# Kernel tuning notes

Measured on AMD Instinct MI355X. Metric: run time of the kernel, lower is better.

## Reference

```python
import jax, jax.numpy as jnp
import numpy as np

C = 256
INTER = C // 8  # 32

def setup_inputs() -> dict:
    key = jax.random.key(0)
    ks = jax.random.split(key, 7)
    B, H, W = 8, 64, 64
    x = jax.random.normal(ks[0], (B, C, H, W), dtype=jnp.float32)
    # 1x1 convs == per-pixel linear maps
    Wq = jax.random.normal(ks[1], (INTER, C), dtype=jnp.float32) * (1.0 / np.sqrt(C))
    bq = jnp.zeros((INTER,), dtype=jnp.float32)
    Wk = jax.random.normal(ks[2], (INTER, C), dtype=jnp.float32) * (1.0 / np.sqrt(C))
    bk = jnp.zeros((INTER,), dtype=jnp.float32)
    Wv = jax.random.normal(ks[3], (C, C), dtype=jnp.float32) * (1.0 / np.sqrt(C))
    bv = jnp.zeros((C,), dtype=jnp.float32)
    gamma = jnp.asarray([0.1], dtype=jnp.float32)  # nonzero so attention path matters
    return {"x": x, "Wq": Wq, "bq": bq, "Wk": Wk, "bk": bk, "Wv": Wv, "bv": bv, "gamma": gamma}

def reference(x, Wq, bq, Wk, bk, Wv, bv, gamma):
    B, Cc, H, W = x.shape
    N = H * W
    xf = x.reshape(B, Cc, N)  # [B, C, N]
    # 1x1 conv projections (per-pixel linear)
    q = jnp.einsum('ic,bcn->bni', Wq, xf) + bq[None, None, :]   # [B, N, inter]
    k = jnp.einsum('ic,bcn->bin', Wk, xf) + bk[None, :, None]   # [B, inter, N]
    v = jnp.einsum('oc,bcn->bon', Wv, xf) + bv[None, :, None]   # [B, C, N]
    energy = jnp.einsum('bni,bim->bnm', q, k)                   # [B, N, N], unscaled
    attn = jax.nn.softmax(energy, axis=-1)                      # softmax over keys
    # out[b,c,i] = sum_j v[b,c,j] * attn[b,i,j]
    out = jnp.einsum('bcj,bij->bci', v, attn).reshape(B, Cc, H, W)
    return gamma[0] * out + x
```

## Files before the change

### kernel.cpp

```cpp
#include <hip/hip_runtime.h>
#include <hip/hip_bf16.h>

#define CCH 256
#define NPIX 4096
#define NB 8
#define LOG2E 1.4426950408889634f

typedef __attribute__((ext_vector_type(8))) short bf16x8;
typedef __attribute__((ext_vector_type(16))) float f32x16;

typedef __attribute__((address_space(3))) unsigned lds_u32;
typedef const __attribute__((address_space(1))) unsigned glb_u32;
#define GL_LDS16(gp, lp) \
    __builtin_amdgcn_global_load_lds((glb_u32*)(gp), (lds_u32*)(lp), 16, 0, 0)

#define PBAR() do { __builtin_amdgcn_sched_barrier(0); \
    asm volatile("s_waitcnt vmcnt(0) lgkmcnt(0)" ::: "memory"); \
    __builtin_amdgcn_s_barrier(); __builtin_amdgcn_sched_barrier(0); } while (0)

static __device__ __forceinline__ unsigned pkbf(float a, float b) {
    union { __hip_bfloat16 h[2]; unsigned u; } p;
    p.h[0] = __float2bfloat16(a);
    p.h[1] = __float2bfloat16(b);
    return p.u;
}
static __device__ __forceinline__ unsigned short bf1(float a) {
    union { __hip_bfloat16 h; unsigned short s; } p;
    p.h = __float2bfloat16(a);
    return p.s;
}

__global__ void packw_kernel(const float* __restrict__ Wq,
                             const float* __restrict__ Wk,
                             const float* __restrict__ Wv,
                             unsigned short* __restrict__ Wb) {
    int i4 = blockIdx.x * 256 + threadIdx.x;
    if (i4 >= 20480) return;
    int e = i4 * 4;
    const float* src;
    if (e < 8192)       src = Wq + e;
    else if (e < 16384) src = Wk + (e - 8192);
    else                src = Wv + (e - 16384);
    float4 v = *(const float4*)src;
    uint2 o;
    o.x = pkbf(v.x, v.y);
    o.y = pkbf(v.z, v.w);
    *(uint2*)(Wb + e) = o;
}

__global__ __launch_bounds__(320) void qkv_kernel(
    const float* __restrict__ x,
    const unsigned short* __restrict__ Wb,
    const float* __restrict__ bq, const float* __restrict__ bk,
    const float* __restrict__ bv,
    unsigned short* __restrict__ q, unsigned short* __restrict__ k,
    unsigned short* __restrict__ v)
{
    __shared__ __align__(16) unsigned xp[128][36];

    const int t   = threadIdx.x;
    const int b   = blockIdx.x >> 7;
    const int px0 = (blockIdx.x & 127) * 32;

    const float4* gx = (const float4*)x + ((size_t)b * CCH * NPIX + px0) / 4;
    for (int i = t; i < 1024; i += 320) {
        int kp = i >> 3, p4 = i & 7;
        float4 lo = gx[(size_t)(2 * kp) * (NPIX / 4) + p4];
        float4 hi = gx[(size_t)(2 * kp + 1) * (NPIX / 4) + p4];
        uint4 pk4;
        pk4.x = pkbf(lo.x, hi.x);
        pk4.y = pkbf(lo.y, hi.y);
        pk4.z = pkbf(lo.z, hi.z);
        pk4.w = pkbf(lo.w, hi.w);
        *(uint4*)&xp[kp][p4 * 4] = pk4;
    }
    __syncthreads();

    const int w  = t >> 6;
    const int lane = t & 63;
    const int qi = lane & 31, h = lane >> 5;

    f32x16 acc[2];
    #pragma unroll
    for (int rt = 0; rt < 2; ++rt)
        #pragma unroll
        for (int r = 0; r < 16; ++r) acc[rt][r] = 0.f;

    #pragma unroll 4
    for (int ks = 0; ks < 16; ++ks) {
        union { unsigned uw[4]; bf16x8 v8; } xb;
        #pragma unroll
        for (int j = 0; j < 4; ++j) xb.uw[j] = xp[ks * 8 + 4 * h + j][qi];
        #pragma unroll
        for (int rt = 0; rt < 2; ++rt) {
            int row = (2 * w + rt) * 32 + qi;
            bf16x8 af = *(const bf16x8*)(Wb + (size_t)row * 256 + ks * 16 + h * 8);
            acc[rt] = __builtin_amdgcn_mfma_f32_32x32x16_bf16(af, xb.v8, acc[rt], 0, 0, 0);
        }
    }

    const int px = px0 + qi;
    const int pxv = px0 + ((qi & 19) | ((qi & 4) << 1) | ((qi & 8) >> 1));
    #pragma unroll
    for (int rt = 0; rt < 2; ++rt) {
        int tile = 2 * w + rt;
        if (tile < 2) {
            const float* bias = (tile == 0) ? bq : bk;
            unsigned short* outp = (tile == 0) ? q : k;
            float scale = (tile == 0) ? LOG2E : 1.0f;
            #pragma unroll
            for (int rg = 0; rg < 4; ++rg) {
                float vv[4];
                #pragma unroll
                for (int j = 0; j < 4; ++j) {
                    int outd = j + 8 * rg + 4 * h;
                    vv[j] = (acc[rt][4 * rg + j] + bias[outd]) * scale;
                }
                uint2 st;
                st.x = pkbf(vv[0], vv[1]);
                st.y = pkbf(vv[2], vv[3]);
                *(uint2*)(outp + ((size_t)b * NPIX + px) * 32 + 8 * rg + 4 * h) = st;
            }
        } else {
            #pragma unroll
            for (int r = 0; r < 16; ++r) {
                int outd = (r & 3) + 8 * (r >> 2) + 4 * h;
                int grow = (tile - 2) * 32 + outd;
                v[((size_t)b * CCH + grow) * NPIX + pxv] = bf1(acc[rt][r] + bv[grow]);
            }
        }
    }
}

__global__ __launch_bounds__(512, 2) void attn_kernel(
    const unsigned short* __restrict__ qg,
    const unsigned short* __restrict__ kg,
    const unsigned short* __restrict__ vg,
    const float* __restrict__ x,
    const float* __restrict__ gamma,
    float* __restrict__ out)
{
    __shared__ __align__(16) unsigned short Kl[2][64][4][8];
    __shared__ __align__(16) unsigned short Vl[2][256][8][8];
    __shared__ __align__(16) unsigned short Pt[2][128][72];
    __shared__ float Lx[128];

    const int t    = threadIdx.x;
    const int b    = blockIdx.x & 7;
    const int n0   = (blockIdx.x >> 3) * 128;
    const int w    = t >> 6;
    const int lane = t & 63;
    const int qi = lane & 31, h = lane >> 5;

    if (w < 4) {
        const int qt = w;
        bf16x8 qf0, qf1;
        {
            const unsigned short* qp = qg + ((size_t)b * NPIX + n0 + qt * 32 + qi) * 32;
            qf0 = *(const bf16x8*)(qp + h * 8);
            qf1 = *(const bf16x8*)(qp + 16 + h * 8);
        }
        const int srow = t >> 2;
        const unsigned short* kg_src =
            kg + ((size_t)b * NPIX + srow) * 32 + ((t & 3) ^ (srow & 3)) * 8;
        char* kl_dst = (char*)Kl + t * 16;
        const unsigned short* krd[2][2];
        #pragma unroll
        for (int sub = 0; sub < 2; ++sub)
            #pragma unroll
            for (int s = 0; s < 2; ++s)
                krd[sub][s] = &Kl[0][sub * 32 + qi][(2 * s + h) ^ (qi & 3)][0];
        unsigned short* pw_base = &Pt[0][32 * qt + qi][4 * h];

        float l_run = 0.f;

        auto STAGEK = [&](int buf, int kt) {
            GL_LDS16(kg_src + (size_t)kt * 2048, kl_dst + buf * 4096);
        };
        auto QKSM = [&](int kt) {
            const int kb = kt & 1;
            f32x16 s0, s1;
            #pragma unroll
            for (int r = 0; r < 16; ++r) { s0[r] = 0.f; s1[r] = 0.f; }
            s0 = __builtin_amdgcn_mfma_f32_32x32x16_bf16(*(const bf16x8*)(krd[0][0] + kb * 2048), qf0, s0, 0, 0, 0);
            s0 = __builtin_amdgcn_mfma_f32_32x32x16_bf16(*(const bf16x8*)(krd[0][1] + kb * 2048), qf1, s0, 0, 0, 0);
            s1 = __builtin_amdgcn_mfma_f32_32x32x16_bf16(*(const bf16x8*)(krd[1][0] + kb * 2048), qf0, s1, 0, 0, 0);
            s1 = __builtin_amdgcn_mfma_f32_32x32x16_bf16(*(const bf16x8*)(krd[1][1] + kb * 2048), qf1, s1, 0, 0, 0);
            unsigned short* pw = pw_base + (kt & 1) * 9216;
            #pragma unroll
            for (int sb = 0; sb < 2; ++sb) {
                const f32x16& sv = sb ? s1 : s0;
                #pragma unroll
                for (int m = 0; m < 4; ++m) {
                    float e0 = exp2f(sv[4 * m + 0]);
                    float e1 = exp2f(sv[4 * m + 1]);
                    float e2 = exp2f(sv[4 * m + 2]);
                    float e3 = exp2f(sv[4 * m + 3]);
                    l_run += (e0 + e1) + (e2 + e3);
                    uint2 val;
                    val.x = pkbf(e0, e1);
                    val.y = pkbf(e2, e3);
                    *(uint2*)(pw + 32 * sb + 8 * m) = val;
                }
            }
        };

        STAGEK(0, 0);
        PBAR();
        QKSM(0);
        STAGEK(1, 1);
        PBAR();
        #pragma unroll 1
        for (int tt = 0; tt < 64; ++tt) {
            if (tt < 63) {
                QKSM(tt + 1);
                if (tt < 62) STAGEK(tt & 1, tt + 2);
            } else {
                float lt = l_run + __shfl_xor(l_run, 32, 64);
                if (lane < 32) Lx[32 * qt + lane] = lt;
            }
            PBAR();
        }
    } else {
        const int cw = w - 4;
        const unsigned short* vg_src =
            vg + ((size_t)b * CCH + 64 * cw + (lane >> 3)) * NPIX +
            ((lane & 7) ^ ((lane >> 3) & 7)) * 8;
        char* vl_dst = (char*)Vl + cw * 8192 + lane * 16;
        const unsigned short* vrd[2][4];
        #pragma unroll
        for (int ct = 0; ct < 2; ++ct)
            #pragma unroll
            for (int s = 0; s < 4; ++s)
                vrd[ct][s] = &Vl[0][64 * cw + 32 * ct + qi][(2 * s + h) ^ (qi & 7)][0];
        const unsigned short* prd = &Pt[0][qi][4 * h];

        f32x16 acc[2][4];
        #pragma unroll
        for (int ct = 0; ct < 2; ++ct)
            #pragma unroll
            for (int qt = 0; qt < 4; ++qt)
                #pragma unroll
                for (int r = 0; r < 16; ++r) acc[ct][qt][r] = 0.f;

        auto STAGEV = [&](int buf, int kt) {
            const unsigned short* s0 = vg_src + kt * 64;
            char* d0 = vl_dst + buf * 32768;
            #pragma unroll
            for (int p = 0; p < 8; ++p)
                GL_LDS16(s0 + (size_t)(8 * p) * NPIX, d0 + p * 1024);
        };
        auto PV = [&](int tt) {
            const int vb = tt & 1;
            bf16x8 vf[2][4];
            #pragma unroll
            for (int ct = 0; ct < 2; ++ct)
                #pragma unroll
                for (int s = 0; s < 4; ++s)
                    vf[ct][s] = *(const bf16x8*)(vrd[ct][s] + vb * 16384);
            const unsigned short* pr0 = prd + (tt & 1) * 9216;
            __builtin_amdgcn_s_setprio(1);
            #pragma unroll
            for (int qt = 0; qt < 4; ++qt) {
                bf16x8 pf[4];
                #pragma unroll
                for (int s = 0; s < 4; ++s) {
                    const unsigned short* pr = pr0 + qt * 2304 + s * 16;
                    uint2 lo = *(const uint2*)(pr);
                    uint2 hi = *(const uint2*)(pr + 8);
                    union { unsigned uw[4]; bf16x8 v8; } pk;
                    pk.uw[0] = lo.x; pk.uw[1] = lo.y;
                    pk.uw[2] = hi.x; pk.uw[3] = hi.y;
                    pf[s] = pk.v8;
                }
                #pragma unroll
                for (int ct = 0; ct < 2; ++ct)
                    #pragma unroll
                    for (int s = 0; s < 4; ++s)
                        acc[ct][qt] = __builtin_amdgcn_mfma_f32_32x32x16_bf16(
                            vf[ct][s], pf[s], acc[ct][qt], 0, 0, 0);
            }
            __builtin_amdgcn_s_setprio(0);
        };

        STAGEV(0, 0);
        PBAR();
        PBAR();
        #pragma unroll 1
        for (int tt = 0; tt < 64; ++tt) {
            if (tt < 63) STAGEV((tt + 1) & 1, tt + 1);
            PV(tt);
            PBAR();
        }

        const float g = gamma[0];
        float rsl[4];
        #pragma unroll
        for (int qt = 0; qt < 4; ++qt) rsl[qt] = g / Lx[32 * qt + qi];
        #pragma unroll
        for (int ct = 0; ct < 2; ++ct) {
            #pragma unroll
            for (int qt = 0; qt < 4; ++qt) {
                #pragma unroll
                for (int r = 0; r < 16; ++r) {
                    int c = 64 * cw + 32 * ct + (r & 3) + 8 * (r >> 2) + 4 * h;
                    size_t off = ((size_t)b * CCH + c) * NPIX + n0 + 32 * qt + qi;
                    out[off] = rsl[qt] * acc[ct][qt][r] + x[off];
                }
            }
        }
    }
}

extern "C" void kernel_launch(void* const* d_in, const int* in_sizes, int n_in,
                              void* d_out, int out_size, void* d_ws, size_t ws_size,
                              hipStream_t stream) {
    const float* x     = (const float*)d_in[0];
    const float* Wq    = (const float*)d_in[1];
    const float* bq    = (const float*)d_in[2];
    const float* Wk    = (const float*)d_in[3];
    const float* bk    = (const float*)d_in[4];
    const float* Wv    = (const float*)d_in[5];
    const float* bv    = (const float*)d_in[6];
    const float* gamma = (const float*)d_in[7];
    float* out = (float*)d_out;

    unsigned short* Wb = (unsigned short*)d_ws;
    unsigned short* qw = Wb + 320 * 256;
    unsigned short* kw = qw + (size_t)NB * NPIX * 32;
    unsigned short* vw = kw + (size_t)NB * NPIX * 32;

    packw_kernel<<<dim3(80), dim3(256), 0, stream>>>(Wq, Wk, Wv, Wb);
    qkv_kernel<<<dim3(NB * (NPIX / 32)), dim3(320), 0, stream>>>(
        x, Wb, bq, bk, bv, qw, kw, vw);
    attn_kernel<<<dim3(256), dim3(512), 0, stream>>>(
        qw, kw, vw, x, gamma, out);
}
```

Baseline: 143.0 us.

## Move V staging to softmax waves and swizzle P tile for 16-byte LDS access

The P tile in shared memory loses its padding and gains an XOR swizzle, so each QK/softmax lane writes a full 16-byte bf16x8 and each PV lane reads one 16-byte vector instead of two 8-byte halves. Global-to-LDS staging of V moves from the PV waves to the QK/softmax waves, which now issue the K and V async copies together at the top of each iteration. This is meant to cut LDS instruction count and bank conflicts and to leave the MFMA-heavy PV waves doing only compute. In exchange the QK waves carry more load traffic, which could lengthen their critical path.

```diff
diff --git a/kernel.cpp b/kernel.cpp
--- a/kernel.cpp
+++ b/kernel.cpp
@@ -142,7 +142,7 @@
 {
     __shared__ __align__(16) unsigned short Kl[2][64][4][8];
     __shared__ __align__(16) unsigned short Vl[2][256][8][8];
-    __shared__ __align__(16) unsigned short Pt[2][128][72];
+    __shared__ __align__(16) unsigned short Pt[2][128][64];
     __shared__ float Lx[128];
 
     const int t    = threadIdx.x;
@@ -151,6 +151,10 @@
     const int w    = t >> 6;
     const int lane = t & 63;
     const int qi = lane & 31, h = lane >> 5;
+
+    int po[4];
+    #pragma unroll
+    for (int s = 0; s < 4; ++s) po[s] = ((2 * s + h) ^ (qi & 7)) * 8;
 
     if (w < 4) {
         const int qt = w;
@@ -163,58 +167,74 @@
         const int srow = t >> 2;
         const unsigned short* kg_src =
             kg + ((size_t)b * NPIX + srow) * 32 + ((t & 3) ^ (srow & 3)) * 8;
+        const int vrow = t >> 3;
+        const unsigned short* vg_src =
+            vg + ((size_t)b * CCH + vrow) * NPIX + ((t & 7) ^ (vrow & 7)) * 8;
         char* kl_dst = (char*)Kl + t * 16;
+        char* vl_dst = (char*)Vl + t * 16;
+
         const unsigned short* krd[2][2];
         #pragma unroll
         for (int sub = 0; sub < 2; ++sub)
             #pragma unroll
             for (int s = 0; s < 2; ++s)
                 krd[sub][s] = &Kl[0][sub * 32 + qi][(2 * s + h) ^ (qi & 3)][0];
-        unsigned short* pw_base = &Pt[0][32 * qt + qi][4 * h];
+        unsigned short* pw = &Pt[0][32 * qt + qi][0];
 
         float l_run = 0.f;
 
-        auto STAGEK = [&](int buf, int kt) {
-            GL_LDS16(kg_src + (size_t)kt * 2048, kl_dst + buf * 4096);
+        auto STAGEV = [&](int kt) {
+            const unsigned short* s0 = vg_src + kt * 64;
+            char* d0 = vl_dst + (kt & 1) * 32768;
+            #pragma unroll
+            for (int p = 0; p < 8; ++p)
+                GL_LDS16(s0 + (size_t)(32 * p) * NPIX, d0 + p * 4096);
+        };
+        auto STAGEK = [&](int kt) {
+            GL_LDS16(kg_src + (size_t)kt * 2048, kl_dst + (kt & 1) * 4096);
         };
         auto QKSM = [&](int kt) {
-            const int kb = kt & 1;
+            const int kb = (kt & 1) * 2048;
             f32x16 s0, s1;
             #pragma unroll
             for (int r = 0; r < 16; ++r) { s0[r] = 0.f; s1[r] = 0.f; }
-            s0 = __builtin_amdgcn_mfma_f32_32x32x16_bf16(*(const bf16x8*)(krd[0][0] + kb * 2048), qf0, s0, 0, 0, 0);
-            s0 = __builtin_amdgcn_mfma_f32_32x32x16_bf16(*(const bf16x8*)(krd[0][1] + kb * 2048), qf1, s0, 0, 0, 0);
-            s1 = __builtin_amdgcn_mfma_f32_32x32x16_bf16(*(const bf16x8*)(krd[1][0] + kb * 2048), qf0, s1, 0, 0, 0);
-            s1 = __builtin_amdgcn_mfma_f32_32x32x16_bf16(*(const bf16x8*)(krd[1][1] + kb * 2048), qf1, s1, 0, 0, 0);
-            unsigned short* pw = pw_base + (kt & 1) * 9216;
-            #pragma unroll
-            for (int sb = 0; sb < 2; ++sb) {
-                const f32x16& sv = sb ? s1 : s0;
-                #pragma unroll
-                for (int m = 0; m < 4; ++m) {
-                    float e0 = exp2f(sv[4 * m + 0]);
-                    float e1 = exp2f(sv[4 * m + 1]);
-                    float e2 = exp2f(sv[4 * m + 2]);
-                    float e3 = exp2f(sv[4 * m + 3]);
-                    l_run += (e0 + e1) + (e2 + e3);
-                    uint2 val;
-                    val.x = pkbf(e0, e1);
-                    val.y = pkbf(e2, e3);
-                    *(uint2*)(pw + 32 * sb + 8 * m) = val;
+            s0 = __builtin_amdgcn_mfma_f32_32x32x16_bf16(*(const bf16x8*)(krd[0][0] + kb), qf0, s0, 0, 0, 0);
+            s0 = __builtin_amdgcn_mfma_f32_32x32x16_bf16(*(const bf16x8*)(krd[0][1] + kb), qf1, s0, 0, 0, 0);
+            s1 = __builtin_amdgcn_mfma_f32_32x32x16_bf16(*(const bf16x8*)(krd[1][0] + kb), qf0, s1, 0, 0, 0);
+            s1 = __builtin_amdgcn_mfma_f32_32x32x16_bf16(*(const bf16x8*)(krd[1][1] + kb), qf1, s1, 0, 0, 0);
+            unsigned short* pwb = pw + (kt & 1) * 8192;
+            #pragma unroll
+            for (int sub = 0; sub < 2; ++sub) {
+                const f32x16& sv = sub ? s1 : s0;
+                #pragma unroll
+                for (int mh = 0; mh < 2; ++mh) {
+                    union { unsigned uw[4]; bf16x8 v8; } pk;
+                    float ps = 0.f;
+                    #pragma unroll
+                    for (int c = 0; c < 4; ++c) {
+                        float ea = exp2f(sv[8 * mh + 2 * c]);
+                        float eb = exp2f(sv[8 * mh + 2 * c + 1]);
+                        ps += ea + eb;
+                        pk.uw[c] = pkbf(ea, eb);
+                    }
+                    l_run += ps;
+                    *(bf16x8*)(pwb + po[2 * sub + mh]) = pk.v8;
                 }
             }
         };
 
-        STAGEK(0, 0);
+        STAGEV(0);
+        STAGEK(0);
+        STAGEK(1);
         PBAR();
         QKSM(0);
-        STAGEK(1, 1);
         PBAR();
         #pragma unroll 1
         for (int tt = 0; tt < 64; ++tt) {
             if (tt < 63) {
+                STAGEV(tt + 1);
+                if (tt < 62) STAGEK(tt + 2);
                 QKSM(tt + 1);
-                if (tt < 62) STAGEK(tt & 1, tt + 2);
             } else {
                 float lt = l_run + __shfl_xor(l_run, 32, 64);
                 if (lane < 32) Lx[32 * qt + lane] = lt;
@@ -223,17 +243,13 @@
         }
     } else {
         const int cw = w - 4;
-        const unsigned short* vg_src =
-            vg + ((size_t)b * CCH + 64 * cw + (lane >> 3)) * NPIX +
-            ((lane & 7) ^ ((lane >> 3) & 7)) * 8;
-        char* vl_dst = (char*)Vl + cw * 8192 + lane * 16;
         const unsigned short* vrd[2][4];
         #pragma unroll
         for (int ct = 0; ct < 2; ++ct)
             #pragma unroll
             for (int s = 0; s < 4; ++s)
                 vrd[ct][s] = &Vl[0][64 * cw + 32 * ct + qi][(2 * s + h) ^ (qi & 7)][0];
-        const unsigned short* prd = &Pt[0][qi][4 * h];
+        const unsigned short* prd = &Pt[0][qi][0];
 
         f32x16 acc[2][4];
         #pragma unroll
@@ -243,36 +259,25 @@
                 #pragma unroll
                 for (int r = 0; r < 16; ++r) acc[ct][qt][r] = 0.f;
 
-        auto STAGEV = [&](int buf, int kt) {
-            const unsigned short* s0 = vg_src + kt * 64;
-            char* d0 = vl_dst + buf * 32768;
-            #pragma unroll
-            for (int p = 0; p < 8; ++p)
-                GL_LDS16(s0 + (size_t)(8 * p) * NPIX, d0 + p * 1024);
-        };
-        auto PV = [&](int tt) {
-            const int vb = tt & 1;
+        PBAR();
+        PBAR();
+        #pragma unroll 1
+        for (int tt = 0; tt < 64; ++tt) {
+            const int vb = (tt & 1) * 16384;
+            const int pb = (tt & 1) * 8192;
             bf16x8 vf[2][4];
             #pragma unroll
             for (int ct = 0; ct < 2; ++ct)
                 #pragma unroll
                 for (int s = 0; s < 4; ++s)
-                    vf[ct][s] = *(const bf16x8*)(vrd[ct][s] + vb * 16384);
-            const unsigned short* pr0 = prd + (tt & 1) * 9216;
+                    vf[ct][s] = *(const bf16x8*)(vrd[ct][s] + vb);
             __builtin_amdgcn_s_setprio(1);
             #pragma unroll
             for (int qt = 0; qt < 4; ++qt) {
                 bf16x8 pf[4];
                 #pragma unroll
-                for (int s = 0; s < 4; ++s) {
-                    const unsigned short* pr = pr0 + qt * 2304 + s * 16;
-                    uint2 lo = *(const uint2*)(pr);
-                    uint2 hi = *(const uint2*)(pr + 8);
-                    union { unsigned uw[4]; bf16x8 v8; } pk;
-                    pk.uw[0] = lo.x; pk.uw[1] = lo.y;
-                    pk.uw[2] = hi.x; pk.uw[3] = hi.y;
-                    pf[s] = pk.v8;
-                }
+                for (int s = 0; s < 4; ++s)
+                    pf[s] = *(const bf16x8*)(prd + pb + qt * 2048 + po[s]);
                 #pragma unroll
                 for (int ct = 0; ct < 2; ++ct)
                     #pragma unroll
@@ -281,15 +286,6 @@
                             vf[ct][s], pf[s], acc[ct][qt], 0, 0, 0);
             }
             __builtin_amdgcn_s_setprio(0);
-        };
-
-        STAGEV(0, 0);
-        PBAR();
-        PBAR();
-        #pragma unroll 1
-        for (int tt = 0; tt < 64; ++tt) {
-            if (tt < 63) STAGEV((tt + 1) & 1, tt + 1);
-            PV(tt);
             PBAR();
         }
 
```

Measured after the change: 141.6 us. Within noise of the previous version (-0.9%).
